# Kernel optimization log

Measured on AMD Instinct MI355X. Metric: run time of the kernel, lower is better.

Reference implementation:

```python
import jax, jax.numpy as jnp
import numpy as np
import math

NUM_ITER = 5
FEAT_STRIDE = 16
GAUSS_SIGMA = 1.0
HINGE_THRESHOLD = -999.0
MIN_FILTER_REG = 1e-3
ALPHA_EPS = 0.0


def apply_filter(feat, weights):
    # feat: (ni, ns, C, H, W); weights: (ns, C, fH, fW) -> scores (ni, ns, oH, oW)
    ni, ns, C, H, W = feat.shape
    fH, fW = weights.shape[-2], weights.shape[-1]
    x = feat.reshape(ni, ns * C, H, W)
    out = jax.lax.conv_general_dilated(
        x, weights, window_strides=(1, 1),
        padding=((fH // 2, fH // 2), (fW // 2, fW // 2)),
        dimension_numbers=('NCHW', 'OIHW', 'NCHW'),
        feature_group_count=ns)
    return out  # (ni, ns, oH, oW); oH = H + (fH+1)%2


def get_label(center, out_sz, sigma):
    # center: (ni, ns, 2) in (row, col) order
    k0 = jnp.arange(out_sz[0], dtype=jnp.float32)[None, None, :, None]
    k1 = jnp.arange(out_sz[1], dtype=jnp.float32)[None, None, None, :]
    g0 = jnp.exp(-0.5 / (sigma * sigma) * (k0 - center[..., 0][..., None, None]) ** 2)
    g1 = jnp.exp(-0.5 / (sigma * sigma) * (k1 - center[..., 1][..., None, None]) ** 2)
    return g0 * g1  # (ni, ns, oH, oW)


def _forward(weights, feat, bb, log_step_length, filter_reg):
    ni, ns = feat.shape[0], feat.shape[1]
    fH, fW = weights.shape[-2], weights.shape[-1]
    out_sz = (feat.shape[-2] + (fH + 1) % 2, feat.shape[-1] + (fW + 1) % 2)
    step = jnp.exp(log_step_length)[0]
    reg = jnp.maximum(filter_reg * filter_reg, MIN_FILTER_REG ** 2)[0]
    dmap_offset = jnp.array([fH % 2, fW % 2], jnp.float32) / 2.0
    # (x, y) -> (row, col), feature-grid coordinates
    center = ((bb[..., :2] + bb[..., 2:] / 2.0) / FEAT_STRIDE)[..., ::-1] - dmap_offset
    label = get_label(center, out_sz, GAUSS_SIGMA)
    mask = (label > HINGE_THRESHOLD).astype(feat.dtype)
    label = label * mask
    sw = math.sqrt(1.0 / ni)

    losses = []
    for _ in range(NUM_ITER):
        scores = apply_filter(feat, weights)
        scores_act = mask * scores + (1.0 - mask) * jax.nn.relu(scores)
        score_mask = mask + (1.0 - mask) * (jax.lax.stop_gradient(scores) > 0).astype(scores.dtype)
        residuals = sw * (scores_act - label)
        losses.append((jnp.sum(residuals ** 2) + reg * jnp.sum(weights ** 2)) / ns)
        residuals_mapped = score_mask * (sw * residuals)
        # feat-transpose = adjoint of apply_filter w.r.t. the filter weights
        _, vjp_fn = jax.vjp(lambda w: apply_filter(feat, w), weights)
        data_grad = vjp_fn(residuals_mapped)[0]
        weights_grad = data_grad + reg * weights
        scores_grad = apply_filter(feat, weights_grad)
        scores_grad = sw * (score_mask * scores_grad)
        alpha_num = jnp.sum(weights_grad ** 2, axis=(1, 2, 3))  # (ns,)
        alpha_den = jnp.maximum(
            jnp.sum(scores_grad.reshape(ni, ns, -1) ** 2, axis=(0, 2))
            + (reg + ALPHA_EPS) * alpha_num, 1e-8)
        alpha = alpha_num / alpha_den
        weights = weights - step * alpha[:, None, None, None] * weights_grad

    scores = apply_filter(feat, weights)
    scores = mask * scores + (1.0 - mask) * jax.nn.relu(scores)
    losses.append((jnp.sum((sw * (scores - label)) ** 2) + reg * jnp.sum(weights ** 2)) / ns)
    return weights, jnp.stack(losses)


def setup_inputs() -> dict:
    key = jax.random.key(0)
    k1, k2, k3, k4 = jax.random.split(key, 4)
    ni, ns, C, H, W, fH, fW = 3, 32, 512, 22, 22, 4, 4
    weights = 0.01 * jax.random.normal(k1, (ns, C, fH, fW), jnp.float32)
    feat = jax.random.normal(k2, (ni, ns, C, H, W), jnp.float32)
    # boxes (x, y, w, h) in image coords (image size = 22*16 = 352)
    xy = jax.random.uniform(k3, (ni, ns, 2), jnp.float32, 50.0, 250.0)
    wh = jax.random.uniform(k4, (ni, ns, 2), jnp.float32, 32.0, 96.0)
    bb = jnp.concatenate([xy, wh], axis=-1)
    log_step_length = jnp.zeros((1,), jnp.float32)  # log(1.0)
    filter_reg = 0.01 * jnp.ones((1,), jnp.float32)
    return {"weights": weights, "feat": feat, "bb": bb,
            "log_step_length": log_step_length, "filter_reg": filter_reg}


def reference(weights, feat, bb, log_step_length, filter_reg):
    return _forward(weights, feat, bb, log_step_length, filter_reg)
```

## Files before the change

### kernel.cpp

```cpp
#include <hip/hip_runtime.h>
#include <hip/hip_fp16.h>

#define NI 3
#define NS 32
#define CHN 512
#define OH 23
#define P2 529
#define NP 50784
#define UV 484
#define WSZ 262144
#define KTOT 1536
#define RSP 1544

typedef unsigned int uint32;
typedef unsigned short u16;
typedef _Float16 h2 __attribute__((ext_vector_type(2)));
typedef _Float16 f16x8 __attribute__((ext_vector_type(8)));
typedef float f32x4 __attribute__((ext_vector_type(4)));

#define OFF_FEATT 0UL
#define OFF_LABEL 47579136UL
#define OFF_S0    47782272UL
#define OFF_S1    47985408UL
#define OFF_SGRAW 48188544UL
#define OFF_WG    48391680UL
#define OFF_WGF16 49440256UL
#define OFF_W0F16 49964544UL
#define OFF_PART  50488832UL
#define OFF_FEATC 50521600UL

#define P_DEN   0
#define P_NUM   4320
#define P_LOSS  5600
#define P_WSQ0  5760
#define P_WSQA  5792
#define P_WSQ5  6816
#define P_L5    7840

__device__ __forceinline__ float waveSum(float v) {
#pragma unroll
  for (int o = 32; o > 0; o >>= 1) v += __shfl_xor(v, o, 64);
  return v;
}

__device__ __forceinline__ float alphaFor(const float* __restrict__ part, int t, int s,
                                          float reg) {
  const float* np_ = part + P_NUM + (size_t)(t * NS + s) * 8;
  const float* dp_ = part + P_DEN + (size_t)(t * NS + s) * 6;
  float nu = 0.f;
#pragma unroll
  for (int i = 0; i < 8; ++i) nu += np_[i];
  float de = 0.f;
#pragma unroll
  for (int i = 0; i < 6; ++i) de += dp_[i];
  return nu / fmaxf(de + reg * nu, 1e-8f);
}

__global__ __launch_bounds__(256) void k_setup(const float* __restrict__ feat,
                                               const float* __restrict__ w0,
                                               const float* __restrict__ bb,
                                               u16* __restrict__ featT,
                                               u16* __restrict__ featC,
                                               u16* __restrict__ w0f16,
                                               float* __restrict__ wmaster,
                                               float* __restrict__ label,
                                               float* __restrict__ part) {
  __shared__ float ldsT[7744];
  __shared__ float sred[4];
  int b = blockIdx.x, tid = threadIdx.x;
  if (b < 3072) {
    int snT = b >> 5, r5 = b & 31;
    int cb = r5 >> 2, uvq = r5 & 3;
    int s = snT / 3, n = snT % 3;
    const float* fsrc =
        feat + ((size_t)n * NS + s) * CHN * UV + (size_t)(cb * 64) * UV + uvq * 121;
#pragma unroll
    for (int it = 0; it < 31; ++it) {
      int idx = it * 256 + tid;
      if (idx < 7744) {
        int r = (unsigned)idx / 121u;
        int j = idx - r * 121;
        ldsT[idx] = fsrc[r * 484 + j];
      }
    }
    __syncthreads();
    uint32* dstb = (uint32*)featT +
                   ((size_t)(snT * 4 + (cb >> 1)) * UV + uvq * 121) * 64 + (cb & 1) * 32;
#pragma unroll
    for (int it = 0; it < 16; ++it) {
      int o = it * 256 + tid;
      if (o < 3872) {
        int uv = o >> 5, k = o & 31;
        float f0 = ldsT[(2 * k) * 121 + uv];
        float f1 = ldsT[(2 * k + 1) * 121 + uv];
        uint32 pk = (uint32)__half_as_ushort(__float2half(f0)) |
                    ((uint32)__half_as_ushort(__float2half(f1)) << 16);
        dstb[(size_t)uv * 64 + k] = pk;
      }
    }
  } else if (b < 3104) {
    int s = b - 3072;
    for (int i = tid; i < 8192; i += 256) {
      int tap = i >> 9, c = i & 511;
      w0f16[(size_t)s * 8192 + i] =
          __half_as_ushort(__float2half(w0[(size_t)s * 8192 + c * 16 + tap]));
    }
    float sq = 0.f;
    for (int i = tid; i < 8192; i += 256) {
      float v = w0[(size_t)s * 8192 + i];
      wmaster[(size_t)s * 8192 + i] = v;
      sq += v * v;
    }
    sq = waveSum(sq);
    if ((tid & 63) == 0) sred[tid >> 6] = sq;
    __syncthreads();
    if (tid == 0) part[P_WSQ0 + s] = sred[0] + sred[1] + sred[2] + sred[3];
  } else if (b < 3303) {
    int p = (b - 3104) * 256 + tid;
    if (p < NP) {
      int nsid = p / P2, rem = p % P2;
      int i = rem / OH, j = rem % OH;
      const float* bp = bb + (size_t)nsid * 4;
      float cr = (bp[1] + 0.5f * bp[3]) * 0.0625f;
      float cc = (bp[0] + 0.5f * bp[2]) * 0.0625f;
      float dy = (float)i - cr, dx = (float)j - cc;
      label[p] = __expf(-0.5f * (dy * dy + dx * dx));
    }
  } else {
    int fb = b - 3303;
    int s = fb / 96;
    int r96 = fb - s * 96;
    int n = r96 >> 5, cg = r96 & 31;
    int c0 = cg * 16;
    const float* srcb = feat + ((size_t)(n * NS + s) * CHN + c0) * UV;
    uint32* dstb = (uint32*)featC + ((size_t)(s * CHN + c0)) * 768 + n * 256;
#pragma unroll
    for (int r = 0; r < 16; ++r) {
      int slot = tid;
      uint32 pk = 0;
      if (slot < 242) {
        float2 v = *(const float2*)(srcb + (size_t)r * UV + 2 * slot);
        pk = (uint32)__half_as_ushort(__float2half(v.x)) |
             ((uint32)__half_as_ushort(__float2half(v.y)) << 16);
      }
      dstb[(size_t)r * 768 + slot] = pk;
    }
  }
}

__global__ __launch_bounds__(1024) void k_conv_fwd(const u16* __restrict__ featT,
                                                   const u16* __restrict__ wf16,
                                                   float* __restrict__ outbuf, int t,
                                                   float* __restrict__ part) {
  __shared__ uint32 w_lds[16 * 260];
  __shared__ float G[288 * 17];
  __shared__ float dred[16];
  int tid = threadIdx.x;
  int bidx = blockIdx.x;
  int snT = bidx >> 1, h = bidx & 1;
  int s = snT / 3, n = snT - s * 3;
  const uint32* wsrc = (const uint32*)(wf16 + (size_t)s * 8192);
  for (int i = tid; i < 4096; i += 1024) {
    int tap = i >> 8, p = i & 255;
    w_lds[tap * 260 + p] = wsrc[i];
  }
  __syncthreads();
  int wave = tid >> 6, lane = tid & 63;
  int q = lane >> 4, m16 = lane & 15;
  int uv0 = h ? 220 : 0;
  int ntiles = 18 - h;
  int t0 = wave;
  bool has2 = (wave + 16 < ntiles);
  int t1 = has2 ? wave + 16 : wave;
  f32x4 acc0 = {0.f, 0.f, 0.f, 0.f}, acc1 = {0.f, 0.f, 0.f, 0.f};
  size_t base = (size_t)snT * 4 * UV * 128;
  int r0i = uv0 + t0 * 16 + m16;
  if (r0i > 483) r0i = 483;
  int r1i = uv0 + t1 * 16 + m16;
  if (r1i > 483) r1i = 483;
  size_t row0 = (size_t)r0i * 128;
  size_t row1 = (size_t)r1i * 128;
#pragma unroll
  for (int step = 0; step < 16; ++step) {
    int cb = step >> 2, cin = (step & 3) * 32;
    size_t cbase = base + (size_t)cb * UV * 128 + cin + q * 8;
    f16x8 a0 = *(const f16x8*)(featT + cbase + row0);
    uint4 bw = *(const uint4*)&w_lds[m16 * 260 + step * 16 + q * 4];
    f16x8 bf = __builtin_bit_cast(f16x8, bw);
    acc0 = __builtin_amdgcn_mfma_f32_16x16x32_f16(a0, bf, acc0, 0, 0, 0);
    if (has2) {
      f16x8 a1 = *(const f16x8*)(featT + cbase + row1);
      acc1 = __builtin_amdgcn_mfma_f32_16x16x32_f16(a1, bf, acc1, 0, 0, 0);
    }
  }
#pragma unroll
  for (int r = 0; r < 4; ++r) G[(t0 * 16 + q * 4 + r) * 17 + m16] = acc0[r];
  if (has2) {
#pragma unroll
    for (int r = 0; r < 4; ++r) G[(t1 * 16 + q * 4 + r) * 17 + m16] = acc1[r];
  }
  __syncthreads();
  float dsq = 0.f;
  int y0 = h ? 12 : 0;
  int npix = h ? 253 : 276;
  int p = tid;
  if (p < npix) {
    int yl = p / 23, x = p - yl * 23;
    int y = y0 + yl;
    float val = 0.f;
#pragma unroll
    for (int ky = 0; ky < 4; ++ky) {
      int u = y + ky - 2;
      if ((unsigned)u < 22u) {
#pragma unroll
        for (int kx = 0; kx < 4; ++kx) {
          int v = x + kx - 2;
          if ((unsigned)v < 22u) val += G[(u * 22 + v - uv0) * 17 + ky * 4 + kx];
        }
      }
    }
    outbuf[(size_t)(n * NS + s) * P2 + y * 23 + x] = val;
    dsq = val * val;
  }
  if (t >= 0) {
    dsq = waveSum(dsq);
    if (lane == 0) dred[wave] = dsq;
    __syncthreads();
    if (tid == 0) {
      float dsum = 0.f;
#pragma unroll
      for (int i = 0; i < 16; ++i) dsum += dred[i];
      part[P_DEN + ((size_t)(t * NS + s) * 3 + n) * 2 + h] = dsum * (1.0f / 3.0f);
    }
  }
}

__global__ __launch_bounds__(512) void k_adjoint(
    int t, const u16* __restrict__ featC, const float* __restrict__ label,
    const float* __restrict__ scores_old, float* __restrict__ scores_new,
    const float* __restrict__ sgraw, float* __restrict__ wg, u16* __restrict__ wgf16,
    float* __restrict__ wmaster, float* __restrict__ part, const float* __restrict__ lsl,
    const float* __restrict__ fr) {
  __shared__ float r_lds[3 * P2];
  __shared__ __align__(16) u16 rs[16 * RSP];
  __shared__ __align__(16) float kred[4][64][4];
  __shared__ float lred[8], nred8[8], wred8[8];
  int tid = threadIdx.x;
  int s = blockIdx.x >> 3, chunk = blockIdx.x & 7;
  int c0 = chunk * 64;
  float step = __expf(lsl[0]);
  float frv = fr[0];
  float reg = fmaxf(frv * frv, 1e-6f);
  float alpha_p = (t >= 1) ? alphaFor(part, t - 1, s, reg) : 0.f;

  float lsum = 0.f;
  for (int pl = tid; pl < 1587; pl += 512) {
    int nn = (unsigned)pl / (unsigned)P2;
    int rem = pl - nn * P2;
    size_t gp = (size_t)(nn * NS + s) * P2 + rem;
    float S = scores_old[gp];
    if (t >= 1) S -= step * alpha_p * sgraw[gp];
    float d = S - label[gp];
    r_lds[nn * P2 + rem] = d * (1.0f / 3.0f);
    if (chunk == 0) {
      if (t >= 1) scores_new[gp] = S;
      lsum += d * d;
    }
  }
  lsum = waveSum(lsum);
  if ((tid & 63) == 0) lred[tid >> 6] = lsum;
  __syncthreads();
  if (chunk == 0 && tid == 0) {
    float L = 0.f;
#pragma unroll
    for (int i = 0; i < 8; ++i) L += lred[i];
    part[P_LOSS + t * NS + s] = L * (1.0f / 3.0f);
  }

  for (int idx = tid; idx < 16 * RSP; idx += 512) {
    int tap = (unsigned)idx / (unsigned)RSP;
    int k = idx - tap * RSP;
    float val = 0.f;
    if (k < KTOT) {
      int n = k >> 9, uv = k & 511;
      if (uv < UV) {
        int u = (unsigned)uv / 22u;
        int v = uv - u * 22;
        int ky = tap >> 2, kx = tap & 3;
        int y = u + 2 - ky, x = v + 2 - kx;
        if ((unsigned)y < 23u && (unsigned)x < 23u) val = r_lds[n * P2 + y * OH + x];
      }
    }
    rs[idx] = __half_as_ushort(__float2half(val));
  }
  __syncthreads();

  int wave = tid >> 6, lane = tid & 63;
  int q = lane >> 4, m16 = lane & 15;
  int tile = wave & 3, khalf = wave >> 2;
  int c = c0 + tile * 16 + m16;
  const u16* arow = featC + ((size_t)(s * CHN + c)) * KTOT + khalf * 768 + q * 8;
  const u16* brow = rs + m16 * RSP + khalf * 768 + q * 8;
  f32x4 acc = {0.f, 0.f, 0.f, 0.f};
#pragma unroll
  for (int ks = 0; ks < 24; ++ks) {
    f16x8 a = *(const f16x8*)(arow + ks * 32);
    f16x8 bf = *(const f16x8*)(brow + ks * 32);
    acc = __builtin_amdgcn_mfma_f32_16x16x32_f16(a, bf, acc, 0, 0, 0);
  }
  if (khalf == 1) *(f32x4*)&kred[tile][lane][0] = acc;
  __syncthreads();

  float num_part = 0.f, wsq_part = 0.f;
  if (khalf == 0) {
    f32x4 o = *(const f32x4*)&kred[tile][lane][0];
    acc += o;
    int tap = m16;
    int ccb = c0 + tile * 16 + q * 4;
    union { u16 h[4]; uint2 v2; } pk;
#pragma unroll
    for (int r = 0; r < 4; ++r) {
      int cc = ccb + r;
      size_t widx = (size_t)s * 8192 + (size_t)cc * 16 + tap;
      float wold = wmaster[widx];
      float wnew = wold;
      if (t >= 1) {
        wnew = wold - step * alpha_p * wg[widx];
        wmaster[widx] = wnew;
      }
      float wgn = acc[r] + reg * wnew;
      wg[widx] = wgn;
      pk.h[r] = __half_as_ushort(__float2half(wgn));
      wsq_part += wnew * wnew;
      num_part += wgn * wgn;
    }
    *(uint2*)&wgf16[(size_t)s * 8192 + (size_t)tap * 512 + ccb] = pk.v2;
  }
  num_part = waveSum(num_part);
  wsq_part = waveSum(wsq_part);
  if (lane == 0) {
    nred8[wave] = num_part;
    wred8[wave] = wsq_part;
  }
  __syncthreads();
  if (tid == 0) {
    float nsum = 0.f, wsum = 0.f;
#pragma unroll
    for (int i = 0; i < 8; ++i) {
      nsum += nred8[i];
      wsum += wred8[i];
    }
    part[P_NUM + (size_t)(t * NS + s) * 8 + chunk] = nsum;
    if (t >= 1) part[P_WSQA + (size_t)((t - 1) * NS + s) * 8 + chunk] = wsum;
  }
}

__global__ void k_final(float* __restrict__ wmaster, const float* __restrict__ wg,
                        const float* __restrict__ scores4, const float* __restrict__ sgraw,
                        const float* __restrict__ label, float* __restrict__ part,
                        const float* __restrict__ lsl, const float* __restrict__ fr) {
  __shared__ float alpha_s[32];
  __shared__ float red4[4];
  int b = blockIdx.x, tid = threadIdx.x;
  float step = __expf(lsl[0]);
  float frv = fr[0];
  float reg = fmaxf(frv * frv, 1e-6f);
  if (tid < 32) alpha_s[tid] = alphaFor(part, 4, tid, reg);
  __syncthreads();
  if (b < 1024) {
    int idx = b * 256 + tid;
    int s = idx >> 13;
    float w5 = wmaster[idx] - step * alpha_s[s] * wg[idx];
    wmaster[idx] = w5;
    float sq = waveSum(w5 * w5);
    if ((tid & 63) == 0) red4[tid >> 6] = sq;
    __syncthreads();
    if (tid == 0) part[P_WSQ5 + b] = red4[0] + red4[1] + red4[2] + red4[3];
  } else {
    int p = (b - 1024) * 256 + tid;
    float contrib = 0.f;
    if (p < NP) {
      int nsid = p / P2;
      int s = nsid & 31;
      float s5 = scores4[p] - step * alpha_s[s] * sgraw[p];
      float d = s5 - label[p];
      contrib = d * d;
    }
    contrib = waveSum(contrib);
    if ((tid & 63) == 0) red4[tid >> 6] = contrib;
    __syncthreads();
    if (tid == 0)
      part[P_L5 + (b - 1024)] = (red4[0] + red4[1] + red4[2] + red4[3]) * (1.0f / 3.0f);
  }
}

__global__ void k_losses(float* __restrict__ out_losses, const float* __restrict__ part,
                         const float* __restrict__ fr) {
  __shared__ float red[8];
  int tid = threadIdx.x;
  float frv = fr[0];
  float reg = fmaxf(frv * frv, 1e-6f);
  float v5 = 0.f;
  for (int i = tid; i < 1024; i += 256) v5 += part[P_WSQ5 + i];
  v5 = waveSum(v5);
  if ((tid & 63) == 0) red[tid >> 6] = v5;
  __syncthreads();
  float wsq5 = red[0] + red[1] + red[2] + red[3];
  float l5 = 0.f;
  for (int i = tid; i < 199; i += 256) l5 += part[P_L5 + i];
  l5 = waveSum(l5);
  if ((tid & 63) == 0) red[4 + (tid >> 6)] = l5;
  __syncthreads();
  float loss5 = red[4] + red[5] + red[6] + red[7];
  if (tid < 5) {
    int t = tid;
    float ls = 0.f;
    for (int i = 0; i < 32; ++i) ls += part[P_LOSS + t * NS + i];
    float ws_ = 0.f;
    if (t == 0) {
      for (int i = 0; i < 32; ++i) ws_ += part[P_WSQ0 + i];
    } else {
      for (int i = 0; i < 256; ++i) ws_ += part[P_WSQA + (t - 1) * 256 + i];
    }
    out_losses[t] = (ls + reg * ws_) * (1.0f / 32.0f);
  }
  if (tid == 5) out_losses[5] = (loss5 + reg * wsq5) * (1.0f / 32.0f);
}

extern "C" void kernel_launch(void* const* d_in, const int* in_sizes, int n_in,
                              void* d_out, int out_size, void* d_ws, size_t ws_size,
                              hipStream_t stream) {
  const float* w0 = (const float*)d_in[0];
  const float* feat = (const float*)d_in[1];
  const float* bb = (const float*)d_in[2];
  const float* lsl = (const float*)d_in[3];
  const float* fr = (const float*)d_in[4];
  float* out = (float*)d_out;
  char* ws = (char*)d_ws;
  u16* featT = (u16*)(ws + OFF_FEATT);
  float* label = (float*)(ws + OFF_LABEL);
  float* s0 = (float*)(ws + OFF_S0);
  float* s1 = (float*)(ws + OFF_S1);
  float* sgraw = (float*)(ws + OFF_SGRAW);
  float* wg = (float*)(ws + OFF_WG);
  u16* wgf16 = (u16*)(ws + OFF_WGF16);
  u16* w0f16 = (u16*)(ws + OFF_W0F16);
  float* part = (float*)(ws + OFF_PART);
  u16* featC = (u16*)(ws + OFF_FEATC);

  k_setup<<<6375, 256, 0, stream>>>(feat, w0, bb, featT, featC, w0f16, out, label, part);
  k_conv_fwd<<<192, 1024, 0, stream>>>(featT, w0f16, s0, -1, part);
  float* sbuf[2] = {s0, s1};
  for (int t = 0; t < 5; ++t) {
    const float* so = (t == 0) ? s0 : sbuf[(t - 1) & 1];
    float* sn = sbuf[t & 1];
    k_adjoint<<<256, 512, 0, stream>>>(t, featC, label, so, sn, sgraw, wg, wgf16, out, part,
                                       lsl, fr);
    k_conv_fwd<<<192, 1024, 0, stream>>>(featT, wgf16, sgraw, t, part);
  }
  k_final<<<1223, 256, 0, stream>>>(out, wg, s0, sgraw, label, part, lsl, fr);
  k_losses<<<1, 256, 0, stream>>>(out + WSZ, part, fr);
}
```

Before: 387.3 us.

## Fuse iteration kernels into one cooperative persistent kernel with grid syncs

```diff
diff --git a/kernel.cpp b/kernel.cpp
--- a/kernel.cpp
+++ b/kernel.cpp
@@ -1,5 +1,8 @@
 #include <hip/hip_runtime.h>
 #include <hip/hip_fp16.h>
+#include <hip/hip_cooperative_groups.h>
+
+namespace cg = cooperative_groups;
 
 #define NI 3
 #define NS 32
@@ -65,7 +68,7 @@
                                                float* __restrict__ wmaster,
                                                float* __restrict__ label,
                                                float* __restrict__ part) {
-  __shared__ float ldsT[7744];
+  __shared__ u16 ldsT[7744];
   __shared__ float sred[4];
   int b = blockIdx.x, tid = threadIdx.x;
   if (b < 3072) {
@@ -80,7 +83,7 @@
       if (idx < 7744) {
         int r = (unsigned)idx / 121u;
         int j = idx - r * 121;
-        ldsT[idx] = fsrc[r * 484 + j];
+        ldsT[idx] = __half_as_ushort(__float2half(fsrc[r * 484 + j]));
       }
     }
     __syncthreads();
@@ -91,10 +94,8 @@
       int o = it * 256 + tid;
       if (o < 3872) {
         int uv = o >> 5, k = o & 31;
-        float f0 = ldsT[(2 * k) * 121 + uv];
-        float f1 = ldsT[(2 * k + 1) * 121 + uv];
-        uint32 pk = (uint32)__half_as_ushort(__float2half(f0)) |
-                    ((uint32)__half_as_ushort(__float2half(f1)) << 16);
+        uint32 pk = (uint32)ldsT[(2 * k) * 121 + uv] |
+                    ((uint32)ldsT[(2 * k + 1) * 121 + uv] << 16);
         dstb[(size_t)uv * 64 + k] = pk;
       }
     }
@@ -148,15 +149,13 @@
   }
 }
 
-__global__ __launch_bounds__(1024) void k_conv_fwd(const u16* __restrict__ featT,
-                                                   const u16* __restrict__ wf16,
-                                                   float* __restrict__ outbuf, int t,
-                                                   float* __restrict__ part) {
-  __shared__ uint32 w_lds[16 * 260];
-  __shared__ float G[288 * 17];
-  __shared__ float dred[16];
-  int tid = threadIdx.x;
-  int bidx = blockIdx.x;
+__device__ __forceinline__ void conv_phase(int bidx, int tid,
+                                           const u16* __restrict__ featT,
+                                           const u16* __restrict__ wf16,
+                                           float* __restrict__ outbuf, int t,
+                                           float* __restrict__ part, uint32* w_lds,
+                                           float* G, float* dred) {
+  if (bidx >= 192) return;
   int snT = bidx >> 1, h = bidx & 1;
   int s = snT / 3, n = snT - s * 3;
   const uint32* wsrc = (const uint32*)(wf16 + (size_t)s * 8192);
@@ -235,18 +234,15 @@
   }
 }
 
-__global__ __launch_bounds__(512) void k_adjoint(
-    int t, const u16* __restrict__ featC, const float* __restrict__ label,
-    const float* __restrict__ scores_old, float* __restrict__ scores_new,
-    const float* __restrict__ sgraw, float* __restrict__ wg, u16* __restrict__ wgf16,
-    float* __restrict__ wmaster, float* __restrict__ part, const float* __restrict__ lsl,
-    const float* __restrict__ fr) {
-  __shared__ float r_lds[3 * P2];
-  __shared__ __align__(16) u16 rs[16 * RSP];
-  __shared__ __align__(16) float kred[4][64][4];
-  __shared__ float lred[8], nred8[8], wred8[8];
-  int tid = threadIdx.x;
-  int s = blockIdx.x >> 3, chunk = blockIdx.x & 7;
+__device__ __forceinline__ void adjoint_phase(
+    int bid, int tid, int t, const u16* __restrict__ featC,
+    const float* __restrict__ label, const float* __restrict__ scores_old,
+    float* __restrict__ scores_new, const float* __restrict__ sgraw,
+    float* __restrict__ wg, u16* __restrict__ wgf16, float* __restrict__ wmaster,
+    float* __restrict__ part, const float* __restrict__ lsl,
+    const float* __restrict__ fr, float* r_lds, u16* rs, float* kred, float* lred,
+    float* nred, float* wred) {
+  int s = bid >> 3, chunk = bid & 7;
   int c0 = chunk * 64;
   float step = __expf(lsl[0]);
   float frv = fr[0];
@@ -254,7 +250,7 @@
   float alpha_p = (t >= 1) ? alphaFor(part, t - 1, s, reg) : 0.f;
 
   float lsum = 0.f;
-  for (int pl = tid; pl < 1587; pl += 512) {
+  for (int pl = tid; pl < 1587; pl += 1024) {
     int nn = (unsigned)pl / (unsigned)P2;
     int rem = pl - nn * P2;
     size_t gp = (size_t)(nn * NS + s) * P2 + rem;
@@ -273,48 +269,49 @@
   if (chunk == 0 && tid == 0) {
     float L = 0.f;
 #pragma unroll
-    for (int i = 0; i < 8; ++i) L += lred[i];
+    for (int i = 0; i < 16; ++i) L += lred[i];
     part[P_LOSS + t * NS + s] = L * (1.0f / 3.0f);
   }
 
-  for (int idx = tid; idx < 16 * RSP; idx += 512) {
-    int tap = (unsigned)idx / (unsigned)RSP;
-    int k = idx - tap * RSP;
-    float val = 0.f;
-    if (k < KTOT) {
-      int n = k >> 9, uv = k & 511;
-      if (uv < UV) {
-        int u = (unsigned)uv / 22u;
-        int v = uv - u * 22;
-        int ky = tap >> 2, kx = tap & 3;
-        int y = u + 2 - ky, x = v + 2 - kx;
-        if ((unsigned)y < 23u && (unsigned)x < 23u) val = r_lds[n * P2 + y * OH + x];
-      }
-    }
-    rs[idx] = __half_as_ushort(__float2half(val));
+  for (int tap = 0; tap < 16; ++tap) {
+    int ky = tap >> 2, kx = tap & 3;
+    for (int k = tid; k < RSP; k += 1024) {
+      float val = 0.f;
+      if (k < KTOT) {
+        int n = k >> 9, uv = k & 511;
+        if (uv < UV) {
+          int u = (unsigned)uv / 22u;
+          int v = uv - u * 22;
+          int y = u + 2 - ky, x = v + 2 - kx;
+          if ((unsigned)y < 23u && (unsigned)x < 23u) val = r_lds[n * P2 + y * OH + x];
+        }
+      }
+      rs[tap * RSP + k] = __half_as_ushort(__float2half(val));
+    }
   }
   __syncthreads();
 
   int wave = tid >> 6, lane = tid & 63;
   int q = lane >> 4, m16 = lane & 15;
-  int tile = wave & 3, khalf = wave >> 2;
+  int tile = wave & 3, kq = wave >> 2;
   int c = c0 + tile * 16 + m16;
-  const u16* arow = featC + ((size_t)(s * CHN + c)) * KTOT + khalf * 768 + q * 8;
-  const u16* brow = rs + m16 * RSP + khalf * 768 + q * 8;
+  const u16* arow = featC + ((size_t)(s * CHN + c)) * KTOT + kq * 384 + q * 8;
+  const u16* brow = rs + m16 * RSP + kq * 384 + q * 8;
   f32x4 acc = {0.f, 0.f, 0.f, 0.f};
 #pragma unroll
-  for (int ks = 0; ks < 24; ++ks) {
+  for (int ks = 0; ks < 12; ++ks) {
     f16x8 a = *(const f16x8*)(arow + ks * 32);
     f16x8 bf = *(const f16x8*)(brow + ks * 32);
     acc = __builtin_amdgcn_mfma_f32_16x16x32_f16(a, bf, acc, 0, 0, 0);
   }
-  if (khalf == 1) *(f32x4*)&kred[tile][lane][0] = acc;
+  if (kq) *(f32x4*)&kred[(((kq - 1) * 4 + tile) * 64 + lane) * 4] = acc;
   __syncthreads();
 
   float num_part = 0.f, wsq_part = 0.f;
-  if (khalf == 0) {
-    f32x4 o = *(const f32x4*)&kred[tile][lane][0];
-    acc += o;
+  if (kq == 0) {
+#pragma unroll
+    for (int kk = 0; kk < 3; ++kk)
+      acc += *(const f32x4*)&kred[((kk * 4 + tile) * 64 + lane) * 4];
     int tap = m16;
     int ccb = c0 + tile * 16 + q * 4;
     union { u16 h[4]; uint2 v2; } pk;
@@ -339,92 +336,122 @@
   num_part = waveSum(num_part);
   wsq_part = waveSum(wsq_part);
   if (lane == 0) {
-    nred8[wave] = num_part;
-    wred8[wave] = wsq_part;
+    nred[wave] = num_part;
+    wred[wave] = wsq_part;
   }
   __syncthreads();
   if (tid == 0) {
     float nsum = 0.f, wsum = 0.f;
 #pragma unroll
-    for (int i = 0; i < 8; ++i) {
-      nsum += nred8[i];
-      wsum += wred8[i];
+    for (int i = 0; i < 16; ++i) {
+      nsum += nred[i];
+      wsum += wred[i];
     }
     part[P_NUM + (size_t)(t * NS + s) * 8 + chunk] = nsum;
     if (t >= 1) part[P_WSQA + (size_t)((t - 1) * NS + s) * 8 + chunk] = wsum;
   }
 }
 
-__global__ void k_final(float* __restrict__ wmaster, const float* __restrict__ wg,
-                        const float* __restrict__ scores4, const float* __restrict__ sgraw,
-                        const float* __restrict__ label, float* __restrict__ part,
-                        const float* __restrict__ lsl, const float* __restrict__ fr) {
+__global__ __launch_bounds__(1024) void k_mega(
+    const u16* __restrict__ featT, const u16* __restrict__ featC,
+    const u16* __restrict__ w0f16, u16* __restrict__ wgf16,
+    const float* __restrict__ label, float* __restrict__ s0, float* __restrict__ s1,
+    float* __restrict__ sgraw, float* __restrict__ wg, float* __restrict__ wmaster,
+    float* __restrict__ part, const float* __restrict__ lsl,
+    const float* __restrict__ fr, float* __restrict__ out_losses) {
+  cg::grid_group grid = cg::this_grid();
+  __shared__ uint32 w_lds[16 * 260];
+  __shared__ float G[288 * 17];
+  __shared__ float dred[16];
+  __shared__ float r_lds[3 * P2];
+  __shared__ __align__(16) u16 rs[16 * RSP];
+  __shared__ __align__(16) float kred[3 * 4 * 64 * 4];
+  __shared__ float lred[16], nred[16], wred[16];
+  __shared__ float redA[16], redB[16];
   __shared__ float alpha_s[32];
-  __shared__ float red4[4];
-  int b = blockIdx.x, tid = threadIdx.x;
-  float step = __expf(lsl[0]);
-  float frv = fr[0];
-  float reg = fmaxf(frv * frv, 1e-6f);
-  if (tid < 32) alpha_s[tid] = alphaFor(part, 4, tid, reg);
-  __syncthreads();
-  if (b < 1024) {
-    int idx = b * 256 + tid;
+  int tid = threadIdx.x, bid = blockIdx.x;
+
+  conv_phase(bid, tid, featT, w0f16, s0, -1, part, w_lds, G, dred);
+  for (int t = 0; t < 5; ++t) {
+    grid.sync();
+    const float* so = (t == 0) ? s0 : (((t - 1) & 1) ? s1 : s0);
+    float* sn = (t & 1) ? s1 : s0;
+    adjoint_phase(bid, tid, t, featC, label, so, sn, sgraw, wg, wgf16, wmaster, part,
+                  lsl, fr, r_lds, rs, kred, lred, nred, wred);
+    grid.sync();
+    conv_phase(bid, tid, featT, wgf16, sgraw, t, part, w_lds, G, dred);
+  }
+  grid.sync();
+
+  {
+    float step = __expf(lsl[0]);
+    float frv = fr[0];
+    float reg = fmaxf(frv * frv, 1e-6f);
+    if (tid < 32) alpha_s[tid] = alphaFor(part, 4, tid, reg);
+    __syncthreads();
+    int idx = bid * 1024 + tid;
     int s = idx >> 13;
     float w5 = wmaster[idx] - step * alpha_s[s] * wg[idx];
     wmaster[idx] = w5;
     float sq = waveSum(w5 * w5);
-    if ((tid & 63) == 0) red4[tid >> 6] = sq;
-    __syncthreads();
-    if (tid == 0) part[P_WSQ5 + b] = red4[0] + red4[1] + red4[2] + red4[3];
-  } else {
-    int p = (b - 1024) * 256 + tid;
+    if ((tid & 63) == 0) redA[tid >> 6] = sq;
     float contrib = 0.f;
-    if (p < NP) {
-      int nsid = p / P2;
-      int s = nsid & 31;
-      float s5 = scores4[p] - step * alpha_s[s] * sgraw[p];
-      float d = s5 - label[p];
-      contrib = d * d;
+    if (bid < 50) {
+      int p = bid * 1024 + tid;
+      if (p < NP) {
+        int nsid = (unsigned)p / (unsigned)P2;
+        int ss = nsid & 31;
+        float s5 = s0[p] - step * alpha_s[ss] * sgraw[p];
+        float d = s5 - label[p];
+        contrib = d * d;
+      }
     }
     contrib = waveSum(contrib);
-    if ((tid & 63) == 0) red4[tid >> 6] = contrib;
-    __syncthreads();
-    if (tid == 0)
-      part[P_L5 + (b - 1024)] = (red4[0] + red4[1] + red4[2] + red4[3]) * (1.0f / 3.0f);
-  }
-}
-
-__global__ void k_losses(float* __restrict__ out_losses, const float* __restrict__ part,
-                         const float* __restrict__ fr) {
-  __shared__ float red[8];
-  int tid = threadIdx.x;
-  float frv = fr[0];
-  float reg = fmaxf(frv * frv, 1e-6f);
-  float v5 = 0.f;
-  for (int i = tid; i < 1024; i += 256) v5 += part[P_WSQ5 + i];
-  v5 = waveSum(v5);
-  if ((tid & 63) == 0) red[tid >> 6] = v5;
-  __syncthreads();
-  float wsq5 = red[0] + red[1] + red[2] + red[3];
-  float l5 = 0.f;
-  for (int i = tid; i < 199; i += 256) l5 += part[P_L5 + i];
-  l5 = waveSum(l5);
-  if ((tid & 63) == 0) red[4 + (tid >> 6)] = l5;
-  __syncthreads();
-  float loss5 = red[4] + red[5] + red[6] + red[7];
-  if (tid < 5) {
-    int t = tid;
-    float ls = 0.f;
-    for (int i = 0; i < 32; ++i) ls += part[P_LOSS + t * NS + i];
-    float ws_ = 0.f;
-    if (t == 0) {
-      for (int i = 0; i < 32; ++i) ws_ += part[P_WSQ0 + i];
-    } else {
-      for (int i = 0; i < 256; ++i) ws_ += part[P_WSQA + (t - 1) * 256 + i];
-    }
-    out_losses[t] = (ls + reg * ws_) * (1.0f / 32.0f);
-  }
-  if (tid == 5) out_losses[5] = (loss5 + reg * wsq5) * (1.0f / 32.0f);
+    if ((tid & 63) == 0) redB[tid >> 6] = contrib;
+    __syncthreads();
+    if (tid == 0) {
+      float a = 0.f, b2 = 0.f;
+#pragma unroll
+      for (int i = 0; i < 16; ++i) {
+        a += redA[i];
+        b2 += redB[i];
+      }
+      part[P_WSQ5 + bid] = a;
+      if (bid < 50) part[P_L5 + bid] = b2 * (1.0f / 3.0f);
+    }
+  }
+  grid.sync();
+
+  if (bid == 0) {
+    float frv = fr[0];
+    float reg = fmaxf(frv * frv, 1e-6f);
+    float v5 = (tid < 256) ? part[P_WSQ5 + tid] : 0.f;
+    v5 = waveSum(v5);
+    if ((tid & 63) == 0) redA[tid >> 6] = v5;
+    float l5 = (tid < 50) ? part[P_L5 + tid] : 0.f;
+    l5 = waveSum(l5);
+    if ((tid & 63) == 0) redB[tid >> 6] = l5;
+    __syncthreads();
+    float wsq5 = 0.f, loss5 = 0.f;
+#pragma unroll
+    for (int i = 0; i < 16; ++i) {
+      wsq5 += redA[i];
+      loss5 += redB[i];
+    }
+    if (tid < 5) {
+      int tt = tid;
+      float ls = 0.f;
+      for (int i = 0; i < 32; ++i) ls += part[P_LOSS + tt * NS + i];
+      float ws_ = 0.f;
+      if (tt == 0) {
+        for (int i = 0; i < 32; ++i) ws_ += part[P_WSQ0 + i];
+      } else {
+        for (int i = 0; i < 256; ++i) ws_ += part[P_WSQA + (tt - 1) * 256 + i];
+      }
+      out_losses[tt] = (ls + reg * ws_) * (1.0f / 32.0f);
+    }
+    if (tid == 5) out_losses[5] = (loss5 + reg * wsq5) * (1.0f / 32.0f);
+  }
 }
 
 extern "C" void kernel_launch(void* const* d_in, const int* in_sizes, int n_in,
@@ -447,17 +474,13 @@
   u16* w0f16 = (u16*)(ws + OFF_W0F16);
   float* part = (float*)(ws + OFF_PART);
   u16* featC = (u16*)(ws + OFF_FEATC);
+  float* lossp = out + WSZ;
 
   k_setup<<<6375, 256, 0, stream>>>(feat, w0, bb, featT, featC, w0f16, out, label, part);
-  k_conv_fwd<<<192, 1024, 0, stream>>>(featT, w0f16, s0, -1, part);
-  float* sbuf[2] = {s0, s1};
-  for (int t = 0; t < 5; ++t) {
-    const float* so = (t == 0) ? s0 : sbuf[(t - 1) & 1];
-    float* sn = sbuf[t & 1];
-    k_adjoint<<<256, 512, 0, stream>>>(t, featC, label, so, sn, sgraw, wg, wgf16, out, part,
-                                       lsl, fr);
-    k_conv_fwd<<<192, 1024, 0, stream>>>(featT, wgf16, sgraw, t, part);
-  }
-  k_final<<<1223, 256, 0, stream>>>(out, wg, s0, sgraw, label, part, lsl, fr);
-  k_losses<<<1, 256, 0, stream>>>(out + WSZ, part, fr);
-}
+  void* args[] = {(void*)&featT, (void*)&featC, (void*)&w0f16, (void*)&wgf16,
+                  (void*)&label, (void*)&s0,    (void*)&s1,    (void*)&sgraw,
+                  (void*)&wg,    (void*)&out,   (void*)&part,  (void*)&lsl,
+                  (void*)&fr,    (void*)&lossp};
+  hipLaunchCooperativeKernel((const void*)k_mega, dim3(256), dim3(1024), args, 0,
+                             stream);
+}
```

Result: slower. 728.7 us (+88.2%).
